# Performance work log

Hardware: AMD Instinct MI355X
Metric: run time of the kernel (lower is better)

Reference implementation:

```python
import jax, jax.numpy as jnp
import numpy as np

BATCH = 16384
N_IN = 128
N_FEAT = N_IN + N_IN * (N_IN + 1) // 2  # 8384
N_OUT = 512


def setup_inputs() -> dict:
    key = jax.random.key(0)
    k1, k2 = jax.random.split(key)
    x = jax.random.normal(k1, (BATCH, N_IN), dtype=jnp.float32)
    # xavier_uniform_ on (in_features, out_features)
    limit = float(np.sqrt(6.0 / (N_FEAT + N_OUT)))
    weight = jax.random.uniform(k2, (N_FEAT, N_OUT), dtype=jnp.float32, minval=-limit, maxval=limit)
    bias = jnp.zeros((N_OUT,), dtype=jnp.float32)
    return {"x": x, "weight": weight, "bias": bias}


def _quadratic_expand(x):
    # Upper-triangle (i<=j) pairwise products in row-major order,
    # matching the torch nested loop (ih, ih+jh).
    n = x.shape[1]
    iu, ju = jnp.triu_indices(n)
    cross = x[:, iu] * x[:, ju]  # [B, n(n+1)/2]
    return jnp.concatenate([x, cross], axis=1)  # [B, n + n(n+1)/2]


def reference(x, weight, bias):
    xc = _quadratic_expand(x)
    return jnp.matmul(xc, weight) + bias
```

## Files before the change

kernel.cpp:

```cpp
#include <hip/hip_runtime.h>

#define NIN    128
#define NOUT   512
#define NBATCH 16384
#define KF     8384
#define KP2    8832
#define NG     (KP2 / 8)
#define NTK2   (KP2 / 64)
#define XSP    136
#define NTK    (KF / 64)
#define XP     136
#define AP     72

typedef float f32x4 __attribute__((ext_vector_type(4)));
typedef __bf16 bf16x8 __attribute__((ext_vector_type(8)));
typedef __bf16 bf16x4 __attribute__((ext_vector_type(4)));

__device__ __forceinline__ int triS(int i) { return (i * (257 - i)) >> 1; }

__global__ void k_tbl(unsigned int* __restrict__ tbl)
{
  int g = blockIdx.x * 256 + threadIdx.x;
  if (g >= NG) return;
  unsigned int e;
  if (g < 16) {
    e = 135u | ((unsigned)(g * 8) << 16);
  } else {
    int gp = g - 16;
    int b = 0;
    #pragma unroll
    for (int bb = 1; bb <= 15; ++bb) {
      int C = 8 * (16 * bb - bb * (bb - 1) / 2);
      if (gp >= C) b = bb;
    }
    int C   = 8 * (16 * b - b * (b - 1) / 2);
    int r   = gp - C;
    int per = 16 - b;
    int i   = 8 * b + r / per;
    int q   = r % per;
    e = (unsigned)i | ((unsigned)(8 * b + 8 * q) << 16);
  }
  tbl[g] = e;
}

__global__ void k_wt2(const float* __restrict__ W,
                      const unsigned int* __restrict__ tbl,
                      __bf16* __restrict__ Wt)
{
  __shared__ __bf16 tile[64][65];
  const int kb   = blockIdx.x >> 3;
  const int nbw  = blockIdx.x & 7;
  const int lane = threadIdx.x & 63;
  const int grp  = threadIdx.x >> 6;
  #pragma unroll 4
  for (int it = 0; it < 16; ++it) {
    int kl = it * 4 + grp;
    int kp = kb * 64 + kl;
    unsigned int e = tbl[kp >> 3];
    int i = (int)(e & 0xFFFFu);
    int j = (int)(e >> 16) + (kp & 7);
    float v = 0.f;
    if (i == 135) {
      v = W[(size_t)kp * NOUT + nbw * 64 + lane];
    } else if (j >= i) {
      int src = 128 + i * 128 - i * (i - 1) / 2 + (j - i);
      v = W[(size_t)src * NOUT + nbw * 64 + lane];
    }
    tile[kl][lane] = (__bf16)v;
  }
  __syncthreads();
  #pragma unroll 4
  for (int it = 0; it < 16; ++it) {
    int nl = it * 4 + grp;
    Wt[(size_t)(nbw * 64 + nl) * KP2 + kb * 64 + lane] = tile[lane][nl];
  }
}

__global__ __launch_bounds__(256, 2) void k_gemm2(
    const float* __restrict__ X,
    const __bf16* __restrict__ Wt,
    const float* __restrict__ bias,
    const unsigned int* __restrict__ tbl,
    float* __restrict__ out)
{
  __shared__ __align__(16) __bf16 xS[128 * XSP];
  __shared__ __align__(16) __bf16 Bt[2][128 * 64];
  __shared__ unsigned int tbl_s[NG];

  const int tid  = threadIdx.x;
  const int lane = tid & 63;
  const int w    = tid >> 6;
  const int mb   = blockIdx.x >> 2;
  const int nb   = blockIdx.x & 3;

  for (int g = tid; g < NG; g += 256) tbl_s[g] = tbl[g];

  {
    const float* xg = X + (size_t)mb * 128 * NIN;
    const int m = tid >> 1, h = tid & 1;
    #pragma unroll
    for (int it = 0; it < 16; ++it) {
      int c4 = h * 64 + it * 4;
      f32x4 v = *reinterpret_cast<const f32x4*>(xg + m * NIN + c4);
      bf16x4 b;
      #pragma unroll
      for (int e = 0; e < 4; ++e) b[e] = (__bf16)v[e];
      *reinterpret_cast<bf16x4*>(&xS[m * XSP + c4]) = b;
    }
    if (tid < 128) xS[tid * XSP + 135] = (__bf16)1.0f;
  }

  const int sn = tid >> 3;
  const int sc = tid & 7;
  const __bf16* wrow = Wt + (size_t)(nb * 128 + sn) * KP2 + sc * 8;
  bf16x8 pf[4];

  f32x4 acc[2][8];
  #pragma unroll
  for (int a = 0; a < 2; ++a)
    #pragma unroll
    for (int b = 0; b < 8; ++b)
      acc[a][b] = f32x4{0.f, 0.f, 0.f, 0.f};

  #pragma unroll
  for (int rep = 0; rep < 4; ++rep)
    pf[rep] = *reinterpret_cast<const bf16x8*>(wrow + (size_t)rep * 32 * KP2);
  #pragma unroll
  for (int rep = 0; rep < 4; ++rep) {
    int n = sn + rep * 32;
    *reinterpret_cast<bf16x8*>(&Bt[0][n * 64 + ((sc ^ (n & 7)) * 8)]) = pf[rep];
  }
  __syncthreads();

  for (int kt = 0; kt < NTK2; ++kt) {
    const int cur = kt & 1;
    if (kt + 1 < NTK2) {
      #pragma unroll
      for (int rep = 0; rep < 4; ++rep)
        pf[rep] = *reinterpret_cast<const bf16x8*>(
            wrow + (size_t)rep * 32 * KP2 + (kt + 1) * 64);
    }

    #pragma unroll
    for (int kh = 0; kh < 2; ++kh) {
      unsigned int e = tbl_s[kt * 8 + kh * 4 + (lane >> 4)];
      const int i  = (int)(e & 0xFFFFu);
      const int j0 = (int)(e >> 16);
      bf16x8 af[2];
      #pragma unroll
      for (int mi = 0; mi < 2; ++mi) {
        int m = w * 32 + mi * 16 + (lane & 15);
        bf16x8 va = *reinterpret_cast<const bf16x8*>(&xS[m * XSP + j0]);
        float sv = (float)xS[m * XSP + i];
        bf16x8 a;
        #pragma unroll
        for (int q = 0; q < 8; ++q) a[q] = (__bf16)(sv * (float)va[q]);
        af[mi] = a;
      }
      const int cb = kh * 4 + (lane >> 4);
      #pragma unroll
      for (int ni = 0; ni < 8; ++ni) {
        int n = ni * 16 + (lane & 15);
        bf16x8 bv = *reinterpret_cast<const bf16x8*>(
            &Bt[cur][n * 64 + ((cb ^ (n & 7)) * 8)]);
        acc[0][ni] = __builtin_amdgcn_mfma_f32_16x16x32_bf16(af[0], bv, acc[0][ni], 0, 0, 0);
        acc[1][ni] = __builtin_amdgcn_mfma_f32_16x16x32_bf16(af[1], bv, acc[1][ni], 0, 0, 0);
      }
    }

    if (kt + 1 < NTK2) {
      #pragma unroll
      for (int rep = 0; rep < 4; ++rep) {
        int n = sn + rep * 32;
        *reinterpret_cast<bf16x8*>(&Bt[cur ^ 1][n * 64 + ((sc ^ (n & 7)) * 8)]) = pf[rep];
      }
    }
    __syncthreads();
  }

  #pragma unroll
  for (int ni = 0; ni < 8; ++ni) {
    int n = nb * 128 + ni * 16 + (lane & 15);
    float bv = bias[n];
    #pragma unroll
    for (int mi = 0; mi < 2; ++mi) {
      int mloc = w * 32 + mi * 16 + ((lane >> 4) << 2);
      #pragma unroll
      for (int q = 0; q < 4; ++q) {
        size_t row = (size_t)mb * 128 + mloc + q;
        out[row * NOUT + n] = acc[mi][ni][q] + bv;
      }
    }
  }
}

__global__ void k_wt(const float* __restrict__ W, __bf16* __restrict__ Wt)
{
  __shared__ __bf16 tile[64][65];
  const int kb   = blockIdx.x >> 3;
  const int nbw  = blockIdx.x & 7;
  const int lane = threadIdx.x & 63;
  const int grp  = threadIdx.x >> 6;
  #pragma unroll 4
  for (int it = 0; it < 16; ++it) {
    int kl = it * 4 + grp;
    tile[kl][lane] = (__bf16)W[(size_t)(kb * 64 + kl) * NOUT + nbw * 64 + lane];
  }
  __syncthreads();
  #pragma unroll 4
  for (int it = 0; it < 16; ++it) {
    int nl = it * 4 + grp;
    Wt[(size_t)(nbw * 64 + nl) * KF + kb * 64 + lane] = tile[lane][nl];
  }
}

template<bool WS>
__global__ __launch_bounds__(256, 2) void k_gemm(
    const float* __restrict__ X, const float* __restrict__ W,
    const __bf16* __restrict__ Wt, const float* __restrict__ bias,
    float* __restrict__ out)
{
  __shared__ __align__(16) __bf16 xT[128 * XP];
  __shared__ __align__(16) __bf16 At[128 * AP];
  __shared__ __align__(16) __bf16 Bt[128 * AP];
  const int tid = threadIdx.x, lane = tid & 63, wid = tid >> 6;
  const int mb = blockIdx.x >> 2, nb = blockIdx.x & 3;
  const int wr = wid >> 1, wc = wid & 1, kk = lane;
  {
    const float* xg = X + (size_t)mb * 128 * 128;
    #pragma unroll
    for (int it = 0; it < 16; ++it) {
      int row = it * 8 + (tid >> 5);
      int c4 = (tid & 31) * 4;
      f32x4 v = *reinterpret_cast<const f32x4*>(xg + row * 128 + c4);
      #pragma unroll
      for (int e = 0; e < 4; ++e) xT[(c4 + e) * XP + row] = (__bf16)v[e];
    }
  }
  f32x4 acc[4][4];
  #pragma unroll
  for (int a = 0; a < 4; ++a)
    #pragma unroll
    for (int b = 0; b < 4; ++b) acc[a][b] = f32x4{0.f, 0.f, 0.f, 0.f};
  __syncthreads();
  for (int kt = 0; kt < NTK; ++kt) {
    if (WS) {
      #pragma unroll
      for (int rep = 0; rep < 4; ++rep) {
        int id = rep * 256 + tid;
        int n = id >> 3, c = id & 7;
        bf16x8 v = *reinterpret_cast<const bf16x8*>(Wt + (size_t)(nb * 128 + n) * KF + kt * 64 + c * 8);
        *reinterpret_cast<bf16x8*>(&Bt[n * AP + c * 8]) = v;
      }
    } else {
      #pragma unroll
      for (int rep = 0; rep < 8; ++rep) {
        int r = rep * 8 + (tid >> 5);
        int cL = (tid & 31) * 4;
        f32x4 wv = *reinterpret_cast<const f32x4*>(W + (size_t)(kt * 64 + r) * NOUT + nb * 128 + cL);
        #pragma unroll
        for (int e = 0; e < 4; ++e) Bt[(cL + e) * AP + r] = (__bf16)wv[e];
      }
    }
    const int k = kt * 64 + kk;
    if (kt >= 2) {
      int idx = k - 128;
      int i = (int)((257.0f - sqrtf((float)(66049 - 8 * idx))) * 0.5f);
      if (i < 0) i = 0;
      if (i > 127) i = 127;
      while (i < 127 && triS(i + 1) <= idx) ++i;
      while (i > 0 && triS(i) > idx) --i;
      int j = i + (idx - triS(i));
      #pragma unroll
      for (int mg = 0; mg < 4; ++mg) {
        int m0 = wid * 32 + mg * 8;
        bf16x8 va = *reinterpret_cast<const bf16x8*>(&xT[i * XP + m0]);
        bf16x8 vb = *reinterpret_cast<const bf16x8*>(&xT[j * XP + m0]);
        #pragma unroll
        for (int q = 0; q < 8; ++q)
          At[(m0 + q) * AP + kk] = (__bf16)((float)va[q] * (float)vb[q]);
      }
    } else {
      #pragma unroll
      for (int mg = 0; mg < 4; ++mg) {
        int m0 = wid * 32 + mg * 8;
        bf16x8 va = *reinterpret_cast<const bf16x8*>(&xT[k * XP + m0]);
        #pragma unroll
        for (int q = 0; q < 8; ++q) At[(m0 + q) * AP + kk] = va[q];
      }
    }
    __syncthreads();
    #pragma unroll
    for (int kh = 0; kh < 2; ++kh) {
      const int koff = kh * 32 + 8 * (lane >> 4);
      bf16x8 af[4], bfv[4];
      #pragma unroll
      for (int mi = 0; mi < 4; ++mi) {
        int m = wr * 64 + mi * 16 + (lane & 15);
        af[mi] = *reinterpret_cast<const bf16x8*>(&At[m * AP + koff]);
      }
      #pragma unroll
      for (int ni = 0; ni < 4; ++ni) {
        int n = wc * 64 + ni * 16 + (lane & 15);
        bfv[ni] = *reinterpret_cast<const bf16x8*>(&Bt[n * AP + koff]);
      }
      #pragma unroll
      for (int mi = 0; mi < 4; ++mi)
        #pragma unroll
        for (int ni = 0; ni < 4; ++ni)
          acc[mi][ni] = __builtin_amdgcn_mfma_f32_16x16x32_bf16(af[mi], bfv[ni], acc[mi][ni], 0, 0, 0);
    }
    __syncthreads();
  }
  #pragma unroll
  for (int ni = 0; ni < 4; ++ni) {
    int n = nb * 128 + wc * 64 + ni * 16 + (lane & 15);
    float bv = bias[n];
    #pragma unroll
    for (int mi = 0; mi < 4; ++mi) {
      int mloc = wr * 64 + mi * 16 + ((lane >> 4) << 2);
      #pragma unroll
      for (int q = 0; q < 4; ++q) {
        size_t row = (size_t)mb * 128 + mloc + q;
        out[row * NOUT + n] = acc[mi][ni][q] + bv;
      }
    }
  }
}

extern "C" void kernel_launch(void* const* d_in, const int* in_sizes, int n_in,
                              void* d_out, int out_size, void* d_ws, size_t ws_size,
                              hipStream_t stream)
{
  const float* X    = (const float*)d_in[0];
  const float* W    = (const float*)d_in[1];
  const float* bias = (const float*)d_in[2];
  float* out        = (float*)d_out;

  const size_t wt2_bytes = (size_t)NOUT * KP2 * 2;
  const size_t need2     = wt2_bytes + (size_t)NG * 4;
  const size_t wt_bytes  = (size_t)NOUT * KF * 2;

  if (d_ws && ws_size >= need2) {
    __bf16* Wt        = (__bf16*)d_ws;
    unsigned int* tbl = (unsigned int*)((char*)d_ws + wt2_bytes);
    k_tbl<<<dim3((NG + 255) / 256), dim3(256), 0, stream>>>(tbl);
    k_wt2<<<dim3(NTK2 * 8), dim3(256), 0, stream>>>(W, tbl, Wt);
    k_gemm2<<<dim3((NBATCH / 128) * 4), dim3(256), 0, stream>>>(X, Wt, bias, tbl, out);
  } else if (d_ws && ws_size >= wt_bytes) {
    __bf16* Wt = (__bf16*)d_ws;
    k_wt<<<dim3(NTK * 8), dim3(256), 0, stream>>>(W, Wt);
    k_gemm<true><<<dim3((NBATCH / 128) * 4), dim3(256), 0, stream>>>(X, W, Wt, bias, out);
  } else {
    k_gemm<false><<<dim3((NBATCH / 128) * 4), dim3(256), 0, stream>>>(X, W, nullptr, bias, out);
  }
}
```

Before: 176.8 us.

## Widen GEMM tile to 128x256 with 2x2 warp grid and single-buffered B

The fused quadratic-expansion GEMM now gives each block a 128x256 output tile instead of 128x128, with a 2x2 wave grid where each wave computes 64x128. This halves the number of blocks that rebuild the A-side pairwise products and share the expanded features. The LDS B tile becomes single-buffered (written before each barrier), and the index table shrinks to 16-bit entries. A bf16 to float conversion done with bit shifts replaces the generic casts. The accumulator count doubles, which raises register pressure and may limit occupancy, and removing double buffering adds a sync stall every k-tile.

```diff
diff --git a/kernel.cpp b/kernel.cpp
--- a/kernel.cpp
+++ b/kernel.cpp
@@ -15,6 +15,7 @@
 typedef float f32x4 __attribute__((ext_vector_type(4)));
 typedef __bf16 bf16x8 __attribute__((ext_vector_type(8)));
 typedef __bf16 bf16x4 __attribute__((ext_vector_type(4)));
+typedef unsigned int u32x4 __attribute__((ext_vector_type(4)));
 
 __device__ __forceinline__ int triS(int i) { return (i * (257 - i)) >> 1; }
 
@@ -76,7 +77,7 @@
   }
 }
 
-__global__ __launch_bounds__(256, 2) void k_gemm2(
+__global__ __launch_bounds__(256, 2) void k_gemm3(
     const float* __restrict__ X,
     const __bf16* __restrict__ Wt,
     const float* __restrict__ bias,
@@ -84,16 +85,21 @@
     float* __restrict__ out)
 {
   __shared__ __align__(16) __bf16 xS[128 * XSP];
-  __shared__ __align__(16) __bf16 Bt[2][128 * 64];
-  __shared__ unsigned int tbl_s[NG];
+  __shared__ __align__(16) __bf16 Bt[256 * 64];
+  __shared__ unsigned short tbl_s[NG];
 
   const int tid  = threadIdx.x;
   const int lane = tid & 63;
-  const int w    = tid >> 6;
-  const int mb   = blockIdx.x >> 2;
-  const int nb   = blockIdx.x & 3;
-
-  for (int g = tid; g < NG; g += 256) tbl_s[g] = tbl[g];
+  const int wid  = tid >> 6;
+  const int wm   = wid >> 1;
+  const int wn   = wid & 1;
+  const int mb   = blockIdx.x >> 1;
+  const int nbb  = blockIdx.x & 1;
+
+  for (int g = tid; g < NG; g += 256) {
+    unsigned int e = tbl[g];
+    tbl_s[g] = (unsigned short)((e & 0xFFu) | ((e >> 16) << 8));
+  }
 
   {
     const float* xg = X + (size_t)mb * 128 * NIN;
@@ -112,67 +118,65 @@
 
   const int sn = tid >> 3;
   const int sc = tid & 7;
-  const __bf16* wrow = Wt + (size_t)(nb * 128 + sn) * KP2 + sc * 8;
-  bf16x8 pf[4];
-
-  f32x4 acc[2][8];
-  #pragma unroll
-  for (int a = 0; a < 2; ++a)
+  const __bf16* wrow = Wt + (size_t)(nbb * 256 + sn) * KP2 + sc * 8;
+  bf16x8 pf[8];
+
+  f32x4 acc[4][8];
+  #pragma unroll
+  for (int a = 0; a < 4; ++a)
     #pragma unroll
     for (int b = 0; b < 8; ++b)
       acc[a][b] = f32x4{0.f, 0.f, 0.f, 0.f};
 
   #pragma unroll
-  for (int rep = 0; rep < 4; ++rep)
+  for (int rep = 0; rep < 8; ++rep)
     pf[rep] = *reinterpret_cast<const bf16x8*>(wrow + (size_t)rep * 32 * KP2);
-  #pragma unroll
-  for (int rep = 0; rep < 4; ++rep) {
-    int n = sn + rep * 32;
-    *reinterpret_cast<bf16x8*>(&Bt[0][n * 64 + ((sc ^ (n & 7)) * 8)]) = pf[rep];
-  }
-  __syncthreads();
 
   for (int kt = 0; kt < NTK2; ++kt) {
-    const int cur = kt & 1;
+    #pragma unroll
+    for (int rep = 0; rep < 8; ++rep) {
+      int n = sn + rep * 32;
+      *reinterpret_cast<bf16x8*>(&Bt[n * 64 + ((sc ^ (n & 7)) * 8)]) = pf[rep];
+    }
+    __syncthreads();
     if (kt + 1 < NTK2) {
       #pragma unroll
-      for (int rep = 0; rep < 4; ++rep)
+      for (int rep = 0; rep < 8; ++rep)
         pf[rep] = *reinterpret_cast<const bf16x8*>(
             wrow + (size_t)rep * 32 * KP2 + (kt + 1) * 64);
     }
 
     #pragma unroll
     for (int kh = 0; kh < 2; ++kh) {
-      unsigned int e = tbl_s[kt * 8 + kh * 4 + (lane >> 4)];
-      const int i  = (int)(e & 0xFFFFu);
-      const int j0 = (int)(e >> 16);
-      bf16x8 af[2];
-      #pragma unroll
-      for (int mi = 0; mi < 2; ++mi) {
-        int m = w * 32 + mi * 16 + (lane & 15);
-        bf16x8 va = *reinterpret_cast<const bf16x8*>(&xS[m * XSP + j0]);
-        float sv = (float)xS[m * XSP + i];
+      unsigned short e = tbl_s[kt * 8 + kh * 4 + (lane >> 4)];
+      const int i  = (int)(e & 0xFFu);
+      const int j0 = (int)(e >> 8);
+      bf16x8 af[4];
+      #pragma unroll
+      for (int mi = 0; mi < 4; ++mi) {
+        int m = wm * 64 + mi * 16 + (lane & 15);
+        u32x4 va = *reinterpret_cast<const u32x4*>(&xS[m * XSP + j0]);
+        unsigned short svu = *reinterpret_cast<const unsigned short*>(&xS[m * XSP + i]);
+        float sv = __builtin_bit_cast(float, (unsigned int)svu << 16);
         bf16x8 a;
         #pragma unroll
-        for (int q = 0; q < 8; ++q) a[q] = (__bf16)(sv * (float)va[q]);
+        for (int q = 0; q < 4; ++q) {
+          float lo = __builtin_bit_cast(float, va[q] << 16);
+          float hi = __builtin_bit_cast(float, va[q] & 0xFFFF0000u);
+          a[2 * q]     = (__bf16)(lo * sv);
+          a[2 * q + 1] = (__bf16)(hi * sv);
+        }
         af[mi] = a;
       }
       const int cb = kh * 4 + (lane >> 4);
       #pragma unroll
       for (int ni = 0; ni < 8; ++ni) {
-        int n = ni * 16 + (lane & 15);
+        int n = wn * 128 + ni * 16 + (lane & 15);
         bf16x8 bv = *reinterpret_cast<const bf16x8*>(
-            &Bt[cur][n * 64 + ((cb ^ (n & 7)) * 8)]);
-        acc[0][ni] = __builtin_amdgcn_mfma_f32_16x16x32_bf16(af[0], bv, acc[0][ni], 0, 0, 0);
-        acc[1][ni] = __builtin_amdgcn_mfma_f32_16x16x32_bf16(af[1], bv, acc[1][ni], 0, 0, 0);
-      }
-    }
-
-    if (kt + 1 < NTK2) {
-      #pragma unroll
-      for (int rep = 0; rep < 4; ++rep) {
-        int n = sn + rep * 32;
-        *reinterpret_cast<bf16x8*>(&Bt[cur ^ 1][n * 64 + ((sc ^ (n & 7)) * 8)]) = pf[rep];
+            &Bt[n * 64 + ((cb ^ (n & 7)) * 8)]);
+        #pragma unroll
+        for (int mi = 0; mi < 4; ++mi)
+          acc[mi][ni] = __builtin_amdgcn_mfma_f32_16x16x32_bf16(af[mi], bv, acc[mi][ni], 0, 0, 0);
       }
     }
     __syncthreads();
@@ -180,11 +184,11 @@
 
   #pragma unroll
   for (int ni = 0; ni < 8; ++ni) {
-    int n = nb * 128 + ni * 16 + (lane & 15);
+    int n = nbb * 256 + wn * 128 + ni * 16 + (lane & 15);
     float bv = bias[n];
     #pragma unroll
-    for (int mi = 0; mi < 2; ++mi) {
-      int mloc = w * 32 + mi * 16 + ((lane >> 4) << 2);
+    for (int mi = 0; mi < 4; ++mi) {
+      int mloc = wm * 64 + mi * 16 + ((lane >> 4) << 2);
       #pragma unroll
       for (int q = 0; q < 4; ++q) {
         size_t row = (size_t)mb * 128 + mloc + q;
@@ -346,7 +350,7 @@
     unsigned int* tbl = (unsigned int*)((char*)d_ws + wt2_bytes);
     k_tbl<<<dim3((NG + 255) / 256), dim3(256), 0, stream>>>(tbl);
     k_wt2<<<dim3(NTK2 * 8), dim3(256), 0, stream>>>(W, tbl, Wt);
-    k_gemm2<<<dim3((NBATCH / 128) * 4), dim3(256), 0, stream>>>(X, Wt, bias, tbl, out);
+    k_gemm3<<<dim3((NBATCH / 128) * 2), dim3(256), 0, stream>>>(X, Wt, bias, tbl, out);
   } else if (d_ws && ws_size >= wt_bytes) {
     __bf16* Wt = (__bf16*)d_ws;
     k_wt<<<dim3(NTK * 8), dim3(256), 0, stream>>>(W, Wt);
```

New measurement: 236.9 us. 34.0% more time.
